# Performance work log

Measured on AMD Instinct MI355X. Metric: run time of the kernel, lower is better.

## Reference

```python
import math
import jax, jax.numpy as jnp
import numpy as np
from jax import lax

# ---- static config (mirrors RPN init + typical torchvision anchor setup) ----
IMG_H = IMG_W = 800
LEVELS = [(200, 200, 4, 32), (100, 100, 8, 64), (50, 50, 16, 128), (25, 25, 32, 256), (13, 13, 64, 512)]  # (h, w, stride, anchor_size)
RATIOS = (0.5, 1.0, 2.0)
COUNTS = tuple(h * w * len(RATIOS) for (h, w, _, _) in LEVELS)  # (120000,30000,7500,1875,507)
A_TOTAL = sum(COUNTS)  # 159882
PRE_NMS = 2000
POST_NMS = 1000
NMS_THRESH = 0.7
MIN_SIZE = 1e-3
BBOX_CLIP = math.log(1000.0 / 16)


def make_anchors():
    parts = []
    for (h, w, stride, size) in LEVELS:
        ws = np.array([size * np.sqrt(1.0 / r) for r in RATIOS], np.float32)  # [3]
        hs = np.array([size * np.sqrt(r) for r in RATIOS], np.float32)
        sx = (np.arange(w, dtype=np.float32) + 0.5) * stride
        sy = (np.arange(h, dtype=np.float32) + 0.5) * stride
        cy, cx = np.meshgrid(sy, sx, indexing='ij')
        cx = cx.reshape(-1, 1)
        cy = cy.reshape(-1, 1)
        a = np.stack([cx - ws / 2, cy - hs / 2, cx + ws / 2, cy + hs / 2], axis=-1)  # [HW,3,4]
        parts.append(a.reshape(-1, 4))
    return np.concatenate(parts, 0).astype(np.float32)


def setup_inputs() -> dict:
    key = jax.random.key(0)
    k1, k2 = jax.random.split(key)
    scores = jax.random.normal(k1, (1, A_TOTAL), dtype=jnp.float32)
    deltas = jax.random.normal(k2, (A_TOTAL, 4), dtype=jnp.float32) * 0.5
    anchors = jnp.asarray(make_anchors())
    return {'scores': scores, 'deltas': deltas, 'anchors': anchors}


def _pairwise_iou(b):
    area = (b[:, 2] - b[:, 0]) * (b[:, 3] - b[:, 1])  # [K]
    lt = jnp.maximum(b[:, None, :2], b[None, :, :2])   # [K,K,2]
    rb = jnp.minimum(b[:, None, 2:], b[None, :, 2:])
    wh = jnp.maximum(rb - lt, 0.0)
    inter = wh[..., 0] * wh[..., 1]
    return inter / (area[:, None] + area[None, :] - inter)


def reference(scores, deltas, anchors):
    s_all = lax.stop_gradient(scores[0])  # original does cls.detach()
    # ---- box decode (torchvision-style) ----
    w = anchors[:, 2] - anchors[:, 0]
    h = anchors[:, 3] - anchors[:, 1]
    cx = anchors[:, 0] + 0.5 * w
    cy = anchors[:, 1] + 0.5 * h
    dx, dy = deltas[:, 0], deltas[:, 1]
    dw = jnp.minimum(deltas[:, 2], BBOX_CLIP)
    dh = jnp.minimum(deltas[:, 3], BBOX_CLIP)
    px = cx + dx * w
    py = cy + dy * h
    pw = jnp.exp(dw) * w
    ph = jnp.exp(dh) * h
    boxes = jnp.stack([px - 0.5 * pw, py - 0.5 * ph, px + 0.5 * pw, py + 0.5 * ph], axis=1)  # [A,4]
    # ---- per-level top-k over objectness ----
    idx_parts = []
    off = 0
    for c in COUNTS:
        k = min(PRE_NMS, c)
        _, ti = lax.top_k(lax.dynamic_slice_in_dim(s_all, off, c), k)
        idx_parts.append(ti + off)
        off += c
    top_idx = jnp.concatenate(idx_parts)  # [K=8382]
    K = top_idx.shape[0]
    s = s_all[top_idx]
    b = boxes[top_idx]
    # ---- clip to image + min-size validity (masked instead of compacted) ----
    b = jnp.stack([jnp.clip(b[:, 0], 0.0, IMG_W), jnp.clip(b[:, 1], 0.0, IMG_H),
                   jnp.clip(b[:, 2], 0.0, IMG_W), jnp.clip(b[:, 3], 0.0, IMG_H)], axis=1)
    valid = ((b[:, 2] - b[:, 0]) >= MIN_SIZE) & ((b[:, 3] - b[:, 1]) >= MIN_SIZE)
    # ---- per-level NMS offset; replicates original feature_mask[keep] indexing
    # (positional indexing into the full anchor-order level-id vector) ----
    fmask_full = np.concatenate([np.full(c, i, np.float32) for i, c in enumerate(COUNTS)])
    fmask = jnp.asarray(fmask_full[:K])
    box_max = jnp.max(jnp.where(valid[:, None], b, -jnp.inf))
    bn = b + (fmask * (box_max + 1.0))[:, None]
    # ---- greedy NMS on score-sorted candidates ----
    s_m = jnp.where(valid, s, -jnp.inf)
    order = jnp.argsort(-s_m)
    s_srt = s_m[order]
    b_srt = b[order]
    iou = _pairwise_iou(bn[order])  # [K,K] ~281MB
    ar = jnp.arange(K)

    def body(i, keep):
        sup = (iou[i] > NMS_THRESH) & (ar > i)
        return jnp.where(keep[i], keep & ~sup, keep)

    keep = lax.fori_loop(0, K, body, s_srt > -jnp.inf)
    final = jnp.where(keep, s_srt, -jnp.inf)
    out_s, oidx = lax.top_k(final, POST_NMS)  # top post_nms kept, score order; -inf pads
    out_b = b_srt[oidx]
    return out_b, out_s
```

## Files before the change

### kernel.cpp

```cpp
#include <hip/hip_runtime.h>
#include <math.h>

typedef unsigned int u32;
typedef unsigned long long u64;
typedef unsigned char u8;

#define K_TOT 8382
#define NCH 131
#define CAP 1024
#define EC 64
#define DC 8
#define GCAP 32768
#define IMGSZ 800.0f

__device__ __constant__ int LOFF[5] = {0, 120000, 150000, 157500, 159375};
__device__ __constant__ int LCNT[5] = {120000, 30000, 7500, 1875, 507};
__device__ __constant__ int KSEL[5] = {2000, 2000, 2000, 1875, 507};
__device__ __constant__ int SELB[5] = {0, 2000, 4000, 6000, 7875};
__device__ __constant__ int HBS[4] = {0, 118, 148, 156};
__device__ __constant__ int GBS[6] = {0, 118, 148, 156, 158, 159};

static __device__ __forceinline__ u32 fkey(float x) {
    u32 u = __float_as_uint(x);
    u32 m = (u32)(((int)u) >> 31) | 0x80000000u;
    return u ^ m;
}

static __device__ __forceinline__ int lvl_of(int s) {
    return (s < 2000) ? 0 : (s < 4000) ? 1 : (s < 6000) ? 2 : (s < 7875) ? 3 : 4;
}

static __device__ __forceinline__ u64 rdlane64(u64 v, int j) {
    u32 lo = (u32)__builtin_amdgcn_readlane((int)(u32)v, j);
    u32 hi = (u32)__builtin_amdgcn_readlane((int)(u32)(v >> 32), j);
    return ((u64)hi << 32) | (u64)lo;
}

static __device__ __forceinline__ void thresh_scan(const u32* hist, u32* scanbuf, int m,
                                                   u32 need, u32* sv, int t) {
    for (int i = t; i < m; i += 1024) scanbuf[i] = hist[m - 1 - i];
    __syncthreads();
    for (int ofs = 1; ofs < m; ofs <<= 1) {
        int i0 = t, i1 = t + 1024;
        u32 a0 = 0, a1 = 0;
        if (i0 < m && i0 >= ofs) a0 = scanbuf[i0 - ofs];
        if (i1 < m && i1 >= ofs) a1 = scanbuf[i1 - ofs];
        __syncthreads();
        if (i0 < m && i0 >= ofs) scanbuf[i0] += a0;
        if (i1 < m && i1 >= ofs) scanbuf[i1] += a1;
        __syncthreads();
    }
    for (int i = t; i < m; i += 1024) {
        u32 inc = scanbuf[i];
        u32 exc = i ? scanbuf[i - 1] : 0;
        if (inc >= need && exc < need) { sv[0] = (u32)(m - 1 - i); sv[1] = need - exc; }
    }
    __syncthreads();
}

__global__ __launch_bounds__(1024) void k_hist(const float* __restrict__ scores,
                                               u32* __restrict__ hist3) {
    __shared__ u32 lh[2048];
    int t = threadIdx.x;
    lh[t] = 0; lh[t + 1024] = 0;
    __syncthreads();
    int b = blockIdx.x;
    int l = (b < HBS[1]) ? 0 : (b < HBS[2]) ? 1 : 2;
    int i = (b - HBS[l]) * 1024 + t;
    if (i < LCNT[l]) atomicAdd(&lh[fkey(scores[LOFF[l] + i]) >> 21], 1u);
    __syncthreads();
    u32* h = hist3 + l * 2048;
    if (lh[t]) atomicAdd(&h[t], lh[t]);
    if (lh[t + 1024]) atomicAdd(&h[t + 1024], lh[t + 1024]);
}

__global__ __launch_bounds__(1024) void k_thresh(const u32* __restrict__ hist3,
                                                 u32* __restrict__ tinfo) {
    __shared__ u32 scanbuf[2048];
    __shared__ u32 sv[2];
    int l = blockIdx.x;
    int t = threadIdx.x;
    thresh_scan(hist3 + l * 2048, scanbuf, 2048, (u32)KSEL[l], sv, t);
    if (t == 0) { tinfo[l * 2] = sv[0]; tinfo[l * 2 + 1] = sv[1]; }
}

__global__ __launch_bounds__(1024) void k_gather(const float* __restrict__ scores,
                                                 const u32* __restrict__ tinfo,
                                                 u32* __restrict__ sel, u32* __restrict__ cgt,
                                                 u32* __restrict__ gcnt, u32* __restrict__ gidx,
                                                 u32* __restrict__ gkey) {
    int b = blockIdx.x;
    int l = (b < GBS[1]) ? 0 : (b < GBS[2]) ? 1 : (b < GBS[3]) ? 2 : (b < GBS[4]) ? 3 : 4;
    int i = (b - GBS[l]) * 1024 + threadIdx.x;
    if (i >= LCNT[l]) return;
    int off = LOFF[l], sb = SELB[l];
    if (l >= 3) { sel[sb + i] = (u32)(off + i); return; }
    u32 ky = fkey(scores[off + i]);
    u32 b1 = tinfo[l * 2];
    u32 top = ky >> 21;
    if (top > b1) {
        u32 p = atomicAdd(&cgt[l], 1u);
        sel[sb + p] = (u32)(off + i);
    } else if (top == b1) {
        u32 e = atomicAdd(&gcnt[l], 1u);
        if (e < GCAP) { gidx[l * GCAP + e] = (u32)i; gkey[l * GCAP + e] = ky; }
    }
}

__global__ __launch_bounds__(1024) void k_final(const u32* __restrict__ gidx,
                                                const u32* __restrict__ gkey,
                                                const u32* __restrict__ gcnt,
                                                const u32* __restrict__ tinfo,
                                                u32* __restrict__ sel) {
    __shared__ u32 hist[2048];
    __shared__ u32 scanbuf[2048];
    __shared__ u32 eqbuf[1024];
    __shared__ u32 sv[2];
    __shared__ u32 c2, ceq;
    int l = blockIdx.x;
    int t = threadIdx.x;
    int k = KSEL[l], sb = SELB[l], off = LOFF[l];
    u32 m = gcnt[l]; if (m > GCAP) m = GCAP;
    u32 b1 = tinfo[l * 2];
    u32 need = tinfo[l * 2 + 1];
    const u32* kb = gkey + l * GCAP;
    const u32* ib = gidx + l * GCAP;
    hist[t] = 0; hist[t + 1024] = 0; __syncthreads();
    for (u32 e = t; e < m; e += 1024) atomicAdd(&hist[(kb[e] >> 10) & 2047u], 1u);
    __syncthreads();
    thresh_scan(hist, scanbuf, 2048, need, sv, t);
    u32 b2 = sv[0], need2 = sv[1];
    __syncthreads();
    hist[t] = 0; __syncthreads();
    for (u32 e = t; e < m; e += 1024) {
        u32 ky = kb[e];
        if (((ky >> 10) & 2047u) == b2) atomicAdd(&hist[ky & 1023u], 1u);
    }
    __syncthreads();
    thresh_scan(hist, scanbuf, 1024, need2, sv, t);
    u32 T = (b1 << 21) | (b2 << 10) | sv[0];
    u32 take = sv[1];
    if (t == 0) { c2 = 0; ceq = 0; }
    __syncthreads();
    u32 nGTbin = need - take;
    u32 base2 = (u32)sb + (u32)k - need;
    for (u32 e = t; e < m; e += 1024) {
        u32 ky = kb[e];
        if (ky > T) { u32 p = atomicAdd(&c2, 1u); sel[base2 + p] = (u32)off + ib[e]; }
        else if (ky == T) { u32 q = atomicAdd(&ceq, 1u); if (q < 1024) eqbuf[q] = ib[e]; }
    }
    __syncthreads();
    if (t == 0) {
        int n = (ceq > 1024u) ? 1024 : (int)ceq;
        for (int a = 1; a < n; ++a) {
            u32 v = eqbuf[a]; int bq = a - 1;
            while (bq >= 0 && eqbuf[bq] > v) { eqbuf[bq + 1] = eqbuf[bq]; --bq; }
            eqbuf[bq + 1] = v;
        }
        for (u32 q = 0; q < take; ++q) sel[base2 + nGTbin + q] = (u32)off + eqbuf[q];
    }
}

__global__ void k_decode(const float* __restrict__ scores, const float4* __restrict__ deltas,
                         const float4* __restrict__ anchors, const u32* __restrict__ sel,
                         float4* __restrict__ candB, float* __restrict__ candS,
                         u32* __restrict__ candV, u32* __restrict__ candA) {
    int s = blockIdx.x * 256 + threadIdx.x;
    if (s >= K_TOT) return;
    u32 a = sel[s];
    float4 an = anchors[a];
    float4 dl = deltas[a];
    float sc = scores[a];
    float w = __fsub_rn(an.z, an.x), h = __fsub_rn(an.w, an.y);
    float cx = __fadd_rn(an.x, __fmul_rn(0.5f, w));
    float cy = __fadd_rn(an.y, __fmul_rn(0.5f, h));
    const float CLIPV = (float)4.1351665567423563;
    float dw = fminf(dl.z, CLIPV);
    float dh = fminf(dl.w, CLIPV);
    float px = __fadd_rn(cx, __fmul_rn(dl.x, w));
    float py = __fadd_rn(cy, __fmul_rn(dl.y, h));
    float pw = __fmul_rn((float)exp((double)dw), w);
    float ph = __fmul_rn((float)exp((double)dh), h);
    float x1 = __fsub_rn(px, __fmul_rn(0.5f, pw));
    float y1 = __fsub_rn(py, __fmul_rn(0.5f, ph));
    float x2 = __fadd_rn(px, __fmul_rn(0.5f, pw));
    float y2 = __fadd_rn(py, __fmul_rn(0.5f, ph));
    x1 = fminf(fmaxf(x1, 0.0f), IMGSZ);
    y1 = fminf(fmaxf(y1, 0.0f), IMGSZ);
    x2 = fminf(fmaxf(x2, 0.0f), IMGSZ);
    y2 = fminf(fmaxf(y2, 0.0f), IMGSZ);
    bool valid = (__fsub_rn(x2, x1) >= 0.001f) && (__fsub_rn(y2, y1) >= 0.001f);
    candB[s] = make_float4(x1, y1, x2, y2);
    candS[s] = sc;
    candV[s] = valid ? 1u : 0u;
    candA[s] = a;
}

__global__ __launch_bounds__(256) void k_rank_lvl(const float* __restrict__ candS,
                                                  const u32* __restrict__ candA,
                                                  u32* __restrict__ Praw) {
    __shared__ u64 tile[256];
    int l = blockIdx.z;
    int cnt = KSEL[l], base = SELB[l];
    int tx = blockIdx.x * 256;
    int ty = blockIdx.y * 256;
    if (tx >= cnt || ty >= cnt) return;
    int t = threadIdx.x;
    u64 Aj = ~0ull;
    if (tx + t < cnt) {
        int j = base + tx + t;
        Aj = ((u64)(~fkey(candS[j])) << 32) | (u64)candA[j];
    }
    tile[t] = Aj;
    __syncthreads();
    int si = ty + t;
    if (si >= cnt) return;
    int s = base + si;
    u64 A = ((u64)(~fkey(candS[s])) << 32) | (u64)candA[s];
    int r = 0;
#pragma unroll 8
    for (int q = 0; q < 256; ++q) r += (tile[q] < A);
    if (r) atomicAdd(&Praw[s], (u32)r);
}

__global__ __launch_bounds__(256) void k_rank_glob(const float* __restrict__ candS,
                                                   const u32* __restrict__ candV,
                                                   const u32* __restrict__ Praw,
                                                   u32* __restrict__ rank) {
    __shared__ u64 colB[256];
    int t = threadIdx.x;
    int cj = blockIdx.x * 256 + t;
    u64 B = ~0ull;
    if (cj < K_TOT) {
        u32 smk = candV[cj] ? fkey(candS[cj]) : 0x007FFFFFu;
        u32 Pj = (u32)SELB[lvl_of(cj)] + Praw[cj];
        B = ((u64)(~smk) << 32) | (u64)Pj;
    }
    colB[t] = B;
    __syncthreads();
    int s = blockIdx.y * 256 + t;
    if (s >= K_TOT) return;
    u32 smk = candV[s] ? fkey(candS[s]) : 0x007FFFFFu;
    u32 Ps = (u32)SELB[lvl_of(s)] + Praw[s];
    u64 myB = ((u64)(~smk) << 32) | (u64)Ps;
    int cnt = 0;
#pragma unroll 8
    for (int j = 0; j < 256; ++j) cnt += (colB[j] < myB);
    if (cnt) atomicAdd(&rank[s], (u32)cnt);
}

__global__ void k_scatter(const float4* __restrict__ candB, const float* __restrict__ candS,
                          const u32* __restrict__ candV, const u32* __restrict__ rank,
                          float4* __restrict__ sB, float* __restrict__ sArea,
                          float* __restrict__ sS, u32* __restrict__ sV) {
    int s = blockIdx.x * 256 + threadIdx.x;
    if (s >= K_TOT) return;
    u32 r = rank[s];
    float4 b = candB[s];
    float area = __fmul_rn(__fsub_rn(b.z, b.x), __fsub_rn(b.w, b.y));
    sB[r] = b; sArea[r] = area; sS[r] = candS[s]; sV[r] = candV[s];
}

__global__ void k_vwords(const u32* __restrict__ sV, u64* __restrict__ vwords) {
    int i = blockIdx.x * 64 + threadIdx.x;
    bool pred = (i < K_TOT) && sV[i];
    u64 bw = __ballot(pred);
    if (threadIdx.x == 0) vwords[blockIdx.x] = bw;
}

__global__ __launch_bounds__(256) void k_mask(const float4* __restrict__ sB,
                                              const float* __restrict__ sArea,
                                              u64* __restrict__ diag, u32* __restrict__ ecnt,
                                              ulonglong2* __restrict__ epack,
                                              u32* __restrict__ dcnt, u64* __restrict__ dmask,
                                              ulonglong2* __restrict__ dpack) {
    __shared__ float4 cb[64];
    __shared__ float ca[64];
    int wd = blockIdx.x;
    int t = threadIdx.x;
    if (t < 64) {
        int j = wd * 64 + t;
        if (j < K_TOT) { cb[t] = sB[j]; ca[t] = sArea[j]; }
        else { cb[t] = make_float4(0.f, 0.f, 0.f, 0.f); ca[t] = 0.f; }
    }
    __syncthreads();
    int i = blockIdx.y * 256 + t;
    if (i >= K_TOT) return;
    int dwr = i >> 6;
    if (wd < dwr) return;
    float4 bi = sB[i];
    float ai = sArea[i];
    u64 bits = 0;
    int jbase = wd * 64;
    for (int j2 = 0; j2 < 64; ++j2) {
        int j = jbase + j2;
        if (j > i && j < K_TOT) {
            float4 bj = cb[j2];
            float ltx = fmaxf(bi.x, bj.x), lty = fmaxf(bi.y, bj.y);
            float rbx = fminf(bi.z, bj.z), rby = fminf(bi.w, bj.w);
            float wx = fmaxf(__fsub_rn(rbx, ltx), 0.0f);
            float wy = fmaxf(__fsub_rn(rby, lty), 0.0f);
            float inter = __fmul_rn(wx, wy);
            if (inter > 0.0f) {
                float uni = __fsub_rn(__fadd_rn(ai, ca[j2]), inter);
                float iou = inter / uni;
                if (iou > 0.7f) bits |= (1ull << j2);
            }
        }
    }
    if (wd == dwr) {
        diag[i] = bits;
        if (bits != 0ull) {
            u32 p = atomicAdd(&dcnt[dwr], 1u);
            if (p < DC) dpack[dwr * DC + p] = make_ulonglong2((u64)(i & 63), bits);
            atomicOr(&dmask[dwr], 1ull << (i & 63));
        }
    } else if (bits != 0ull) {
        u32 p = atomicAdd(&ecnt[dwr], 1u);
        if (p < CAP) epack[dwr * CAP + p] = make_ulonglong2((u64)((i & 63) | (wd << 6)), bits);
    }
}

__global__ __launch_bounds__(64) void k_scan(const u64* __restrict__ diag,
                                             const u64* __restrict__ vwords,
                                             const u32* __restrict__ ecnt,
                                             const ulonglong2* __restrict__ epack,
                                             const u32* __restrict__ dcnt,
                                             const u64* __restrict__ dmask,
                                             const ulonglong2* __restrict__ dpack,
                                             u64* __restrict__ keepw) {
    __shared__ u64 sVw[NCH];
    __shared__ u32 sCnt[NCH];
    __shared__ u32 sDn[NCH];
    __shared__ u64 sDm[NCH];
    __shared__ ulonglong2 sEpack[NCH * EC];
    __shared__ ulonglong2 sDpack[NCH * DC];
    volatile __shared__ u64 sR[NCH];
    __shared__ u64 sKeep[NCH];
    int lane = threadIdx.x;
    {
        int i0 = lane, i1 = lane + 64, i2 = lane + 128;
        bool p2 = (i2 < NCH);
        u64 v0 = vwords[i0], v1 = vwords[i1], v2 = p2 ? vwords[i2] : 0;
        u32 c0 = ecnt[i0], c1 = ecnt[i1], c2 = p2 ? ecnt[i2] : 0;
        u32 d0 = dcnt[i0], d1 = dcnt[i1], d2 = p2 ? dcnt[i2] : 0;
        u64 m0 = dmask[i0], m1 = dmask[i1], m2 = p2 ? dmask[i2] : 0;
        sVw[i0] = v0; sCnt[i0] = (c0 > CAP) ? CAP : c0; sDn[i0] = d0; sDm[i0] = m0; sR[i0] = 0;
        sVw[i1] = v1; sCnt[i1] = (c1 > CAP) ? CAP : c1; sDn[i1] = d1; sDm[i1] = m1; sR[i1] = 0;
        if (p2) { sVw[i2] = v2; sCnt[i2] = (c2 > CAP) ? CAP : c2; sDn[i2] = d2; sDm[i2] = m2; sR[i2] = 0; }
    }
    for (int base = 0; base < NCH; base += 16) {
        ulonglong2 tmp[16];
        int nb = NCH - base; if (nb > 16) nb = 16;
#pragma unroll
        for (int b = 0; b < 16; ++b)
            if (b < nb) tmp[b] = epack[(size_t)(base + b) * CAP + lane];
#pragma unroll
        for (int b = 0; b < 16; ++b)
            if (b < nb) sEpack[(base + b) * EC + lane] = tmp[b];
    }
    for (int base = 0; base < NCH * DC; base += 64 * 8) {
        ulonglong2 tmp[8];
#pragma unroll
        for (int b = 0; b < 8; ++b) {
            int i = base + b * 64 + lane;
            if (i < NCH * DC) tmp[b] = dpack[i];
        }
#pragma unroll
        for (int b = 0; b < 8; ++b) {
            int i = base + b * 64 + lane;
            if (i < NCH * DC) sDpack[i] = tmp[b];
        }
    }
    __syncthreads();
    for (int c = 0; c < NCH; ++c) {
        u32 cnt = sCnt[c];
        u32 dn = sDn[c];
        ulonglong2 E = sEpack[c * EC + lane];
        ulonglong2 DP = (lane < DC) ? sDpack[c * DC + lane] : make_ulonglong2(~0ull, 0ull);
        u64 vw = sVw[c];
        u64 alive = vw & ~sR[c];
        if (dn) {
            if (dn <= (u32)DC) {
                u64 dm = sDm[c];
                u32 ml = ((u32)lane < dn) ? (u32)DP.x : 0xFFu;
                while (dm) {
                    int j = __builtin_ctzll(dm);
                    dm &= dm - 1;
                    if ((alive >> j) & 1ull) {
                        u64 selm = __ballot(ml == (u32)j);
                        int src = __builtin_ctzll(selm);
                        alive &= ~rdlane64(DP.y, src);
                    }
                }
            } else {
                int r = c * 64 + lane;
                u64 D = (r < K_TOT) ? diag[r] : 0ull;
                u64 nzd = __ballot(D != 0ull);
                while (nzd) {
                    int j = __builtin_ctzll(nzd);
                    nzd &= nzd - 1;
                    if ((alive >> j) & 1ull) alive &= ~rdlane64(D, j);
                }
            }
        }
        if (lane == 0) sKeep[c] = alive;
        if ((u32)lane < cnt && ((alive >> ((u32)E.x & 63u)) & 1ull))
            atomicOr((u64*)&sR[(u32)E.x >> 6], E.y);
        if (cnt > (u32)EC) {
            for (u32 e = (u32)EC + (u32)lane; e < cnt; e += 64u) {
                ulonglong2 Et = epack[(size_t)c * CAP + e];
                u32 pk = (u32)Et.x;
                if ((alive >> (pk & 63u)) & 1ull) atomicOr((u64*)&sR[pk >> 6], Et.y);
            }
        }
    }
    __syncthreads();
    for (int i = lane; i < NCH; i += 64) keepw[i] = sKeep[i];
}

__global__ __launch_bounds__(1024) void k_out(const u64* __restrict__ keepw,
                                              const float4* __restrict__ sB,
                                              const float* __restrict__ sS,
                                              float* __restrict__ out) {
    __shared__ u32 wpre[NCH + 1];
    int t = threadIdx.x;
    if (t == 0) {
        u32 run = 0;
        for (int w = 0; w < NCH; ++w) { wpre[w] = run; run += (u32)__popcll(keepw[w]); }
        wpre[NCH] = run;
    }
    __syncthreads();
    u32 nk = wpre[NCH];
    for (int i = t; i < K_TOT; i += 1024) {
        int w = i >> 6, b = i & 63;
        u64 kw = keepw[w];
        u32 kb = wpre[w] + (u32)__popcll(kw & ((1ull << b) - 1ull));
        bool kp = (kw >> b) & 1ull;
        if (kp) {
            if (kb < 1000u) {
                float4 bx = sB[i];
                out[kb * 4 + 0] = bx.x; out[kb * 4 + 1] = bx.y;
                out[kb * 4 + 2] = bx.z; out[kb * 4 + 3] = bx.w;
                out[4000 + kb] = sS[i];
            }
        } else {
            u32 q = (u32)i - kb;
            u32 slot = nk + q;
            if (slot < 1000u) {
                float4 bx = sB[i];
                out[slot * 4 + 0] = bx.x; out[slot * 4 + 1] = bx.y;
                out[slot * 4 + 2] = bx.z; out[slot * 4 + 3] = bx.w;
                out[4000 + slot] = -INFINITY;
            }
        }
    }
}

static constexpr size_t al256(size_t x) { return (x + 255) & ~(size_t)255; }
static constexpr size_t KB4 = (size_t)K_TOT * 4;
static constexpr size_t KB16 = (size_t)K_TOT * 16;
static constexpr size_t O_RANK = 0;
static constexpr size_t O_PRAW = al256(O_RANK + KB4);
static constexpr size_t O_ECNT = al256(O_PRAW + KB4);
static constexpr size_t O_DCNT = al256(O_ECNT + (size_t)NCH * 4);
static constexpr size_t O_DMASK = al256(O_DCNT + (size_t)NCH * 4);
static constexpr size_t O_HIST = al256(O_DMASK + (size_t)NCH * 8);
static constexpr size_t O_CGT = al256(O_HIST + (size_t)3 * 2048 * 4);
static constexpr size_t O_GCNT = al256(O_CGT + 3 * 4);
static constexpr size_t MEMSET_BYTES = al256(O_GCNT + 3 * 4);
static constexpr size_t O_TINFO = MEMSET_BYTES;
static constexpr size_t O_SEL = al256(O_TINFO + 6 * 4);
static constexpr size_t O_GIDX = al256(O_SEL + KB4);
static constexpr size_t O_GKEY = al256(O_GIDX + (size_t)3 * GCAP * 4);
static constexpr size_t O_CANDB = al256(O_GKEY + (size_t)3 * GCAP * 4);
static constexpr size_t O_CANDS = al256(O_CANDB + KB16);
static constexpr size_t O_CANDV = al256(O_CANDS + KB4);
static constexpr size_t O_CANDA = al256(O_CANDV + KB4);
static constexpr size_t O_SB = al256(O_CANDA + KB4);
static constexpr size_t O_SAREA = al256(O_SB + KB16);
static constexpr size_t O_SS = al256(O_SAREA + KB4);
static constexpr size_t O_SV = al256(O_SS + KB4);
static constexpr size_t O_VW = al256(O_SV + KB4);
static constexpr size_t O_KW = al256(O_VW + (size_t)NCH * 8);
static constexpr size_t O_DIAG = al256(O_KW + (size_t)NCH * 8);
static constexpr size_t O_EPACK = al256(O_DIAG + (size_t)(NCH * 64) * 8);
static constexpr size_t O_DPACK = al256(O_EPACK + (size_t)NCH * CAP * 16);

extern "C" void kernel_launch(void* const* d_in, const int* in_sizes, int n_in,
                              void* d_out, int out_size, void* d_ws, size_t ws_size,
                              hipStream_t stream) {
    const float* scores = (const float*)d_in[0];
    const float4* deltas = (const float4*)d_in[1];
    const float4* anchors = (const float4*)d_in[2];
    float* out = (float*)d_out;
    char* ws = (char*)d_ws;

    u32* rank = (u32*)(ws + O_RANK);
    u32* Praw = (u32*)(ws + O_PRAW);
    u32* ecnt = (u32*)(ws + O_ECNT);
    u32* dcnt = (u32*)(ws + O_DCNT);
    u64* dmask = (u64*)(ws + O_DMASK);
    u32* hist3 = (u32*)(ws + O_HIST);
    u32* cgt = (u32*)(ws + O_CGT);
    u32* gcnt = (u32*)(ws + O_GCNT);
    u32* tinfo = (u32*)(ws + O_TINFO);
    u32* sel = (u32*)(ws + O_SEL);
    u32* gidx = (u32*)(ws + O_GIDX);
    u32* gkey = (u32*)(ws + O_GKEY);
    float4* candB = (float4*)(ws + O_CANDB);
    float* candS = (float*)(ws + O_CANDS);
    u32* candV = (u32*)(ws + O_CANDV);
    u32* candA = (u32*)(ws + O_CANDA);
    float4* sB = (float4*)(ws + O_SB);
    float* sArea = (float*)(ws + O_SAREA);
    float* sS = (float*)(ws + O_SS);
    u32* sV = (u32*)(ws + O_SV);
    u64* vwords = (u64*)(ws + O_VW);
    u64* keepw = (u64*)(ws + O_KW);
    u64* diag = (u64*)(ws + O_DIAG);
    ulonglong2* epack = (ulonglong2*)(ws + O_EPACK);
    ulonglong2* dpack = (ulonglong2*)(ws + O_DPACK);

    hipMemsetAsync(ws, 0, MEMSET_BYTES, stream);

    const int NBLK = (K_TOT + 255) / 256;
    k_hist<<<156, 1024, 0, stream>>>(scores, hist3);
    k_thresh<<<3, 1024, 0, stream>>>(hist3, tinfo);
    k_gather<<<159, 1024, 0, stream>>>(scores, tinfo, sel, cgt, gcnt, gidx, gkey);
    k_final<<<3, 1024, 0, stream>>>(gidx, gkey, gcnt, tinfo, sel);
    k_decode<<<NBLK, 256, 0, stream>>>(scores, deltas, anchors, sel, candB, candS, candV, candA);
    k_rank_lvl<<<dim3(8, 8, 5), 256, 0, stream>>>(candS, candA, Praw);
    k_rank_glob<<<dim3(NBLK, NBLK), 256, 0, stream>>>(candS, candV, Praw, rank);
    k_scatter<<<NBLK, 256, 0, stream>>>(candB, candS, candV, rank, sB, sArea, sS, sV);
    k_vwords<<<NCH, 64, 0, stream>>>(sV, vwords);
    k_mask<<<dim3(NCH, NBLK), 256, 0, stream>>>(sB, sArea, diag, ecnt, epack, dcnt, dmask, dpack);
    k_scan<<<1, 64, 0, stream>>>(diag, vwords, ecnt, epack, dcnt, dmask, dpack, keepw);
    k_out<<<1, 1024, 0, stream>>>(keepw, sB, sS, out);
}
```

Before: 226.0 us.

## Fuse selection stages via last-block tickets and merge rank passes into one

Folds the threshold scan into the histogram kernel and the final refinement into the gather kernel, using an atomic ticket so the last block to finish does the serial work. This removes two launches. The per-level rank kernel is replaced by a lexicographic two-key comparison inside the global rank kernel, and the valid-word ballot moves into the mask kernel. The scan kernel now keeps per-chunk metadata in registers read through readlane instead of shared memory. The cost is serialized tail work on a single block and a heavier inner compare loop in the rank kernel.

```diff
diff --git a/kernel.cpp b/kernel.cpp
--- a/kernel.cpp
+++ b/kernel.cpp
@@ -59,8 +59,12 @@
 }
 
 __global__ __launch_bounds__(1024) void k_hist(const float* __restrict__ scores,
-                                               u32* __restrict__ hist3) {
+                                               u32* __restrict__ hist3,
+                                               u32* __restrict__ tinfo,
+                                               u32* __restrict__ ticket) {
     __shared__ u32 lh[2048];
+    __shared__ u32 sv[2];
+    __shared__ u32 lastF;
     int t = threadIdx.x;
     lh[t] = 0; lh[t + 1024] = 0;
     __syncthreads();
@@ -72,92 +76,100 @@
     u32* h = hist3 + l * 2048;
     if (lh[t]) atomicAdd(&h[t], lh[t]);
     if (lh[t + 1024]) atomicAdd(&h[t + 1024], lh[t + 1024]);
-}
-
-__global__ __launch_bounds__(1024) void k_thresh(const u32* __restrict__ hist3,
-                                                 u32* __restrict__ tinfo) {
-    __shared__ u32 scanbuf[2048];
-    __shared__ u32 sv[2];
-    int l = blockIdx.x;
-    int t = threadIdx.x;
-    thresh_scan(hist3 + l * 2048, scanbuf, 2048, (u32)KSEL[l], sv, t);
-    if (t == 0) { tinfo[l * 2] = sv[0]; tinfo[l * 2 + 1] = sv[1]; }
+    __threadfence();
+    __syncthreads();
+    if (t == 0) lastF = (atomicAdd(ticket, 1u) == 155u) ? 1u : 0u;
+    __syncthreads();
+    if (!lastF) return;
+    __threadfence();
+    for (int lv = 0; lv < 3; ++lv) {
+        thresh_scan(hist3 + lv * 2048, lh, 2048, (u32)KSEL[lv], sv, t);
+        if (t == 0) { tinfo[lv * 2] = sv[0]; tinfo[lv * 2 + 1] = sv[1]; }
+        __syncthreads();
+    }
 }
 
 __global__ __launch_bounds__(1024) void k_gather(const float* __restrict__ scores,
                                                  const u32* __restrict__ tinfo,
                                                  u32* __restrict__ sel, u32* __restrict__ cgt,
                                                  u32* __restrict__ gcnt, u32* __restrict__ gidx,
-                                                 u32* __restrict__ gkey) {
-    int b = blockIdx.x;
-    int l = (b < GBS[1]) ? 0 : (b < GBS[2]) ? 1 : (b < GBS[3]) ? 2 : (b < GBS[4]) ? 3 : 4;
-    int i = (b - GBS[l]) * 1024 + threadIdx.x;
-    if (i >= LCNT[l]) return;
-    int off = LOFF[l], sb = SELB[l];
-    if (l >= 3) { sel[sb + i] = (u32)(off + i); return; }
-    u32 ky = fkey(scores[off + i]);
-    u32 b1 = tinfo[l * 2];
-    u32 top = ky >> 21;
-    if (top > b1) {
-        u32 p = atomicAdd(&cgt[l], 1u);
-        sel[sb + p] = (u32)(off + i);
-    } else if (top == b1) {
-        u32 e = atomicAdd(&gcnt[l], 1u);
-        if (e < GCAP) { gidx[l * GCAP + e] = (u32)i; gkey[l * GCAP + e] = ky; }
-    }
-}
-
-__global__ __launch_bounds__(1024) void k_final(const u32* __restrict__ gidx,
-                                                const u32* __restrict__ gkey,
-                                                const u32* __restrict__ gcnt,
-                                                const u32* __restrict__ tinfo,
-                                                u32* __restrict__ sel) {
+                                                 u32* __restrict__ gkey,
+                                                 u32* __restrict__ ticket) {
     __shared__ u32 hist[2048];
     __shared__ u32 scanbuf[2048];
     __shared__ u32 eqbuf[1024];
     __shared__ u32 sv[2];
     __shared__ u32 c2, ceq;
-    int l = blockIdx.x;
+    __shared__ u32 lastF;
     int t = threadIdx.x;
-    int k = KSEL[l], sb = SELB[l], off = LOFF[l];
-    u32 m = gcnt[l]; if (m > GCAP) m = GCAP;
-    u32 b1 = tinfo[l * 2];
-    u32 need = tinfo[l * 2 + 1];
-    const u32* kb = gkey + l * GCAP;
-    const u32* ib = gidx + l * GCAP;
-    hist[t] = 0; hist[t + 1024] = 0; __syncthreads();
-    for (u32 e = t; e < m; e += 1024) atomicAdd(&hist[(kb[e] >> 10) & 2047u], 1u);
-    __syncthreads();
-    thresh_scan(hist, scanbuf, 2048, need, sv, t);
-    u32 b2 = sv[0], need2 = sv[1];
-    __syncthreads();
-    hist[t] = 0; __syncthreads();
-    for (u32 e = t; e < m; e += 1024) {
-        u32 ky = kb[e];
-        if (((ky >> 10) & 2047u) == b2) atomicAdd(&hist[ky & 1023u], 1u);
-    }
-    __syncthreads();
-    thresh_scan(hist, scanbuf, 1024, need2, sv, t);
-    u32 T = (b1 << 21) | (b2 << 10) | sv[0];
-    u32 take = sv[1];
-    if (t == 0) { c2 = 0; ceq = 0; }
-    __syncthreads();
-    u32 nGTbin = need - take;
-    u32 base2 = (u32)sb + (u32)k - need;
-    for (u32 e = t; e < m; e += 1024) {
-        u32 ky = kb[e];
-        if (ky > T) { u32 p = atomicAdd(&c2, 1u); sel[base2 + p] = (u32)off + ib[e]; }
-        else if (ky == T) { u32 q = atomicAdd(&ceq, 1u); if (q < 1024) eqbuf[q] = ib[e]; }
-    }
-    __syncthreads();
-    if (t == 0) {
-        int n = (ceq > 1024u) ? 1024 : (int)ceq;
-        for (int a = 1; a < n; ++a) {
-            u32 v = eqbuf[a]; int bq = a - 1;
-            while (bq >= 0 && eqbuf[bq] > v) { eqbuf[bq + 1] = eqbuf[bq]; --bq; }
-            eqbuf[bq + 1] = v;
-        }
-        for (u32 q = 0; q < take; ++q) sel[base2 + nGTbin + q] = (u32)off + eqbuf[q];
+    int b = blockIdx.x;
+    int l = (b < GBS[1]) ? 0 : (b < GBS[2]) ? 1 : (b < GBS[3]) ? 2 : (b < GBS[4]) ? 3 : 4;
+    int i = (b - GBS[l]) * 1024 + t;
+    if (i < LCNT[l]) {
+        int off = LOFF[l], sb = SELB[l];
+        if (l >= 3) {
+            sel[sb + i] = (u32)(off + i);
+        } else {
+            u32 ky = fkey(scores[off + i]);
+            u32 b1 = tinfo[l * 2];
+            u32 top = ky >> 21;
+            if (top > b1) {
+                u32 p = atomicAdd(&cgt[l], 1u);
+                sel[sb + p] = (u32)(off + i);
+            } else if (top == b1) {
+                u32 e = atomicAdd(&gcnt[l], 1u);
+                if (e < GCAP) { gidx[l * GCAP + e] = (u32)i; gkey[l * GCAP + e] = ky; }
+            }
+        }
+    }
+    __threadfence();
+    __syncthreads();
+    if (t == 0) lastF = (atomicAdd(ticket, 1u) == 158u) ? 1u : 0u;
+    __syncthreads();
+    if (!lastF) return;
+    __threadfence();
+    for (int lv = 0; lv < 3; ++lv) {
+        int k = KSEL[lv], sb = SELB[lv], off = LOFF[lv];
+        u32 m = gcnt[lv]; if (m > GCAP) m = GCAP;
+        u32 b1 = tinfo[lv * 2];
+        u32 need = tinfo[lv * 2 + 1];
+        const u32* kb = gkey + lv * GCAP;
+        const u32* ib = gidx + lv * GCAP;
+        hist[t] = 0; hist[t + 1024] = 0; __syncthreads();
+        for (u32 e = t; e < m; e += 1024) atomicAdd(&hist[(kb[e] >> 10) & 2047u], 1u);
+        __syncthreads();
+        thresh_scan(hist, scanbuf, 2048, need, sv, t);
+        u32 b2 = sv[0], need2 = sv[1];
+        __syncthreads();
+        hist[t] = 0; __syncthreads();
+        for (u32 e = t; e < m; e += 1024) {
+            u32 ky = kb[e];
+            if (((ky >> 10) & 2047u) == b2) atomicAdd(&hist[ky & 1023u], 1u);
+        }
+        __syncthreads();
+        thresh_scan(hist, scanbuf, 1024, need2, sv, t);
+        u32 T = (b1 << 21) | (b2 << 10) | sv[0];
+        u32 take = sv[1];
+        if (t == 0) { c2 = 0; ceq = 0; }
+        __syncthreads();
+        u32 nGTbin = need - take;
+        u32 base2 = (u32)sb + (u32)k - need;
+        for (u32 e = t; e < m; e += 1024) {
+            u32 ky = kb[e];
+            if (ky > T) { u32 p = atomicAdd(&c2, 1u); sel[base2 + p] = (u32)off + ib[e]; }
+            else if (ky == T) { u32 q = atomicAdd(&ceq, 1u); if (q < 1024) eqbuf[q] = ib[e]; }
+        }
+        __syncthreads();
+        if (t == 0) {
+            int n = (ceq > 1024u) ? 1024 : (int)ceq;
+            for (int a = 1; a < n; ++a) {
+                u32 v = eqbuf[a]; int bq = a - 1;
+                while (bq >= 0 && eqbuf[bq] > v) { eqbuf[bq + 1] = eqbuf[bq]; --bq; }
+                eqbuf[bq + 1] = v;
+            }
+            for (u32 q = 0; q < take; ++q) sel[base2 + nGTbin + q] = (u32)off + eqbuf[q];
+        }
+        __syncthreads();
     }
 }
 
@@ -196,56 +208,35 @@
     candA[s] = a;
 }
 
-__global__ __launch_bounds__(256) void k_rank_lvl(const float* __restrict__ candS,
-                                                  const u32* __restrict__ candA,
-                                                  u32* __restrict__ Praw) {
-    __shared__ u64 tile[256];
-    int l = blockIdx.z;
-    int cnt = KSEL[l], base = SELB[l];
-    int tx = blockIdx.x * 256;
-    int ty = blockIdx.y * 256;
-    if (tx >= cnt || ty >= cnt) return;
-    int t = threadIdx.x;
-    u64 Aj = ~0ull;
-    if (tx + t < cnt) {
-        int j = base + tx + t;
-        Aj = ((u64)(~fkey(candS[j])) << 32) | (u64)candA[j];
-    }
-    tile[t] = Aj;
-    __syncthreads();
-    int si = ty + t;
-    if (si >= cnt) return;
-    int s = base + si;
-    u64 A = ((u64)(~fkey(candS[s])) << 32) | (u64)candA[s];
-    int r = 0;
-#pragma unroll 8
-    for (int q = 0; q < 256; ++q) r += (tile[q] < A);
-    if (r) atomicAdd(&Praw[s], (u32)r);
-}
-
 __global__ __launch_bounds__(256) void k_rank_glob(const float* __restrict__ candS,
                                                    const u32* __restrict__ candV,
-                                                   const u32* __restrict__ Praw,
+                                                   const u32* __restrict__ candA,
                                                    u32* __restrict__ rank) {
-    __shared__ u64 colB[256];
+    __shared__ u64 cA1[256];
+    __shared__ u64 cA2[256];
     int t = threadIdx.x;
     int cj = blockIdx.x * 256 + t;
-    u64 B = ~0ull;
+    u64 a1 = ~0ull, a2 = ~0ull;
     if (cj < K_TOT) {
-        u32 smk = candV[cj] ? fkey(candS[cj]) : 0x007FFFFFu;
-        u32 Pj = (u32)SELB[lvl_of(cj)] + Praw[cj];
-        B = ((u64)(~smk) << 32) | (u64)Pj;
-    }
-    colB[t] = B;
+        u32 kyj = fkey(candS[cj]);
+        u32 smk = candV[cj] ? kyj : 0x007FFFFFu;
+        a1 = ((u64)(~smk) << 32) | (u64)lvl_of(cj);
+        a2 = ((u64)(~kyj) << 32) | (u64)candA[cj];
+    }
+    cA1[t] = a1; cA2[t] = a2;
     __syncthreads();
     int s = blockIdx.y * 256 + t;
     if (s >= K_TOT) return;
-    u32 smk = candV[s] ? fkey(candS[s]) : 0x007FFFFFu;
-    u32 Ps = (u32)SELB[lvl_of(s)] + Praw[s];
-    u64 myB = ((u64)(~smk) << 32) | (u64)Ps;
+    u32 kys = fkey(candS[s]);
+    u32 smk = candV[s] ? kys : 0x007FFFFFu;
+    u64 m1 = ((u64)(~smk) << 32) | (u64)lvl_of(s);
+    u64 m2 = ((u64)(~kys) << 32) | (u64)candA[s];
     int cnt = 0;
-#pragma unroll 8
-    for (int j = 0; j < 256; ++j) cnt += (colB[j] < myB);
+#pragma unroll 4
+    for (int j = 0; j < 256; ++j) {
+        u64 t1 = cA1[j];
+        cnt += (t1 < m1) || (t1 == m1 && cA2[j] < m2);
+    }
     if (cnt) atomicAdd(&rank[s], (u32)cnt);
 }
 
@@ -261,23 +252,24 @@
     sB[r] = b; sArea[r] = area; sS[r] = candS[s]; sV[r] = candV[s];
 }
 
-__global__ void k_vwords(const u32* __restrict__ sV, u64* __restrict__ vwords) {
-    int i = blockIdx.x * 64 + threadIdx.x;
-    bool pred = (i < K_TOT) && sV[i];
-    u64 bw = __ballot(pred);
-    if (threadIdx.x == 0) vwords[blockIdx.x] = bw;
-}
-
 __global__ __launch_bounds__(256) void k_mask(const float4* __restrict__ sB,
                                               const float* __restrict__ sArea,
+                                              const u32* __restrict__ sV,
                                               u64* __restrict__ diag, u32* __restrict__ ecnt,
                                               ulonglong2* __restrict__ epack,
                                               u32* __restrict__ dcnt, u64* __restrict__ dmask,
-                                              ulonglong2* __restrict__ dpack) {
+                                              ulonglong2* __restrict__ dpack,
+                                              u64* __restrict__ vwords) {
     __shared__ float4 cb[64];
     __shared__ float ca[64];
     int wd = blockIdx.x;
     int t = threadIdx.x;
+    if (blockIdx.y == 0 && t < 64) {
+        int j = wd * 64 + t;
+        bool pred = (j < K_TOT) && (sV[j] != 0u);
+        u64 bw = __ballot(pred);
+        if (t == 0) vwords[wd] = bw;
+    }
     if (t < 64) {
         int j = wd * 64 + t;
         if (j < K_TOT) { cb[t] = sB[j]; ca[t] = sArea[j]; }
@@ -329,26 +321,19 @@
                                              const u64* __restrict__ dmask,
                                              const ulonglong2* __restrict__ dpack,
                                              u64* __restrict__ keepw) {
-    __shared__ u64 sVw[NCH];
-    __shared__ u32 sCnt[NCH];
-    __shared__ u32 sDn[NCH];
-    __shared__ u64 sDm[NCH];
     __shared__ ulonglong2 sEpack[NCH * EC];
     __shared__ ulonglong2 sDpack[NCH * DC];
     volatile __shared__ u64 sR[NCH];
     __shared__ u64 sKeep[NCH];
     int lane = threadIdx.x;
-    {
-        int i0 = lane, i1 = lane + 64, i2 = lane + 128;
-        bool p2 = (i2 < NCH);
-        u64 v0 = vwords[i0], v1 = vwords[i1], v2 = p2 ? vwords[i2] : 0;
-        u32 c0 = ecnt[i0], c1 = ecnt[i1], c2 = p2 ? ecnt[i2] : 0;
-        u32 d0 = dcnt[i0], d1 = dcnt[i1], d2 = p2 ? dcnt[i2] : 0;
-        u64 m0 = dmask[i0], m1 = dmask[i1], m2 = p2 ? dmask[i2] : 0;
-        sVw[i0] = v0; sCnt[i0] = (c0 > CAP) ? CAP : c0; sDn[i0] = d0; sDm[i0] = m0; sR[i0] = 0;
-        sVw[i1] = v1; sCnt[i1] = (c1 > CAP) ? CAP : c1; sDn[i1] = d1; sDm[i1] = m1; sR[i1] = 0;
-        if (p2) { sVw[i2] = v2; sCnt[i2] = (c2 > CAP) ? CAP : c2; sDn[i2] = d2; sDm[i2] = m2; sR[i2] = 0; }
-    }
+    int i0 = lane, i1 = lane + 64, i2 = lane + 128;
+    bool p2 = (i2 < NCH);
+    u64 vwR0 = vwords[i0], vwR1 = vwords[i1], vwR2 = p2 ? vwords[i2] : 0;
+    u32 cR0 = ecnt[i0], cR1 = ecnt[i1], cR2 = p2 ? ecnt[i2] : 0;
+    u32 dR0 = dcnt[i0], dR1 = dcnt[i1], dR2 = p2 ? dcnt[i2] : 0;
+    u64 mR0 = dmask[i0], mR1 = dmask[i1], mR2 = p2 ? dmask[i2] : 0;
+    cR0 = (cR0 > CAP) ? CAP : cR0; cR1 = (cR1 > CAP) ? CAP : cR1; cR2 = (cR2 > CAP) ? CAP : cR2;
+    sR[i0] = 0; sR[i1] = 0; if (p2) sR[i2] = 0;
     for (int base = 0; base < NCH; base += 16) {
         ulonglong2 tmp[16];
         int nb = NCH - base; if (nb > 16) nb = 16;
@@ -374,19 +359,31 @@
     }
     __syncthreads();
     for (int c = 0; c < NCH; ++c) {
-        u32 cnt = sCnt[c];
-        u32 dn = sDn[c];
+        int g = c >> 6, l = c & 63;
+        u64 vw, dm; u32 cnt, dn;
+        if (g == 0) {
+            vw = rdlane64(vwR0, l); dm = rdlane64(mR0, l);
+            cnt = (u32)__builtin_amdgcn_readlane((int)cR0, l);
+            dn = (u32)__builtin_amdgcn_readlane((int)dR0, l);
+        } else if (g == 1) {
+            vw = rdlane64(vwR1, l); dm = rdlane64(mR1, l);
+            cnt = (u32)__builtin_amdgcn_readlane((int)cR1, l);
+            dn = (u32)__builtin_amdgcn_readlane((int)dR1, l);
+        } else {
+            vw = rdlane64(vwR2, l); dm = rdlane64(mR2, l);
+            cnt = (u32)__builtin_amdgcn_readlane((int)cR2, l);
+            dn = (u32)__builtin_amdgcn_readlane((int)dR2, l);
+        }
         ulonglong2 E = sEpack[c * EC + lane];
         ulonglong2 DP = (lane < DC) ? sDpack[c * DC + lane] : make_ulonglong2(~0ull, 0ull);
-        u64 vw = sVw[c];
         u64 alive = vw & ~sR[c];
         if (dn) {
             if (dn <= (u32)DC) {
-                u64 dm = sDm[c];
                 u32 ml = ((u32)lane < dn) ? (u32)DP.x : 0xFFu;
-                while (dm) {
-                    int j = __builtin_ctzll(dm);
-                    dm &= dm - 1;
+                u64 dmm = dm;
+                while (dmm) {
+                    int j = __builtin_ctzll(dmm);
+                    dmm &= dmm - 1;
                     if ((alive >> j) & 1ull) {
                         u64 selm = __ballot(ml == (u32)j);
                         int src = __builtin_ctzll(selm);
@@ -461,14 +458,14 @@
 static constexpr size_t KB4 = (size_t)K_TOT * 4;
 static constexpr size_t KB16 = (size_t)K_TOT * 16;
 static constexpr size_t O_RANK = 0;
-static constexpr size_t O_PRAW = al256(O_RANK + KB4);
-static constexpr size_t O_ECNT = al256(O_PRAW + KB4);
+static constexpr size_t O_ECNT = al256(O_RANK + KB4);
 static constexpr size_t O_DCNT = al256(O_ECNT + (size_t)NCH * 4);
 static constexpr size_t O_DMASK = al256(O_DCNT + (size_t)NCH * 4);
 static constexpr size_t O_HIST = al256(O_DMASK + (size_t)NCH * 8);
 static constexpr size_t O_CGT = al256(O_HIST + (size_t)3 * 2048 * 4);
 static constexpr size_t O_GCNT = al256(O_CGT + 3 * 4);
-static constexpr size_t MEMSET_BYTES = al256(O_GCNT + 3 * 4);
+static constexpr size_t O_TK = al256(O_GCNT + 3 * 4);
+static constexpr size_t MEMSET_BYTES = al256(O_TK + 2 * 4);
 static constexpr size_t O_TINFO = MEMSET_BYTES;
 static constexpr size_t O_SEL = al256(O_TINFO + 6 * 4);
 static constexpr size_t O_GIDX = al256(O_SEL + KB4);
@@ -497,13 +494,13 @@
     char* ws = (char*)d_ws;
 
     u32* rank = (u32*)(ws + O_RANK);
-    u32* Praw = (u32*)(ws + O_PRAW);
     u32* ecnt = (u32*)(ws + O_ECNT);
     u32* dcnt = (u32*)(ws + O_DCNT);
     u64* dmask = (u64*)(ws + O_DMASK);
     u32* hist3 = (u32*)(ws + O_HIST);
     u32* cgt = (u32*)(ws + O_CGT);
     u32* gcnt = (u32*)(ws + O_GCNT);
+    u32* ticket = (u32*)(ws + O_TK);
     u32* tinfo = (u32*)(ws + O_TINFO);
     u32* sel = (u32*)(ws + O_SEL);
     u32* gidx = (u32*)(ws + O_GIDX);
@@ -522,19 +519,16 @@
     ulonglong2* epack = (ulonglong2*)(ws + O_EPACK);
     ulonglong2* dpack = (ulonglong2*)(ws + O_DPACK);
 
-    hipMemsetAsync(ws, 0, MEMSET_BYTES, stream);
+    (void)hipMemsetAsync(ws, 0, MEMSET_BYTES, stream);
 
     const int NBLK = (K_TOT + 255) / 256;
-    k_hist<<<156, 1024, 0, stream>>>(scores, hist3);
-    k_thresh<<<3, 1024, 0, stream>>>(hist3, tinfo);
-    k_gather<<<159, 1024, 0, stream>>>(scores, tinfo, sel, cgt, gcnt, gidx, gkey);
-    k_final<<<3, 1024, 0, stream>>>(gidx, gkey, gcnt, tinfo, sel);
+    k_hist<<<156, 1024, 0, stream>>>(scores, hist3, tinfo, &ticket[0]);
+    k_gather<<<159, 1024, 0, stream>>>(scores, tinfo, sel, cgt, gcnt, gidx, gkey, &ticket[1]);
     k_decode<<<NBLK, 256, 0, stream>>>(scores, deltas, anchors, sel, candB, candS, candV, candA);
-    k_rank_lvl<<<dim3(8, 8, 5), 256, 0, stream>>>(candS, candA, Praw);
-    k_rank_glob<<<dim3(NBLK, NBLK), 256, 0, stream>>>(candS, candV, Praw, rank);
+    k_rank_glob<<<dim3(NBLK, NBLK), 256, 0, stream>>>(candS, candV, candA, rank);
     k_scatter<<<NBLK, 256, 0, stream>>>(candB, candS, candV, rank, sB, sArea, sS, sV);
-    k_vwords<<<NCH, 64, 0, stream>>>(sV, vwords);
-    k_mask<<<dim3(NCH, NBLK), 256, 0, stream>>>(sB, sArea, diag, ecnt, epack, dcnt, dmask, dpack);
+    k_mask<<<dim3(NCH, NBLK), 256, 0, stream>>>(sB, sArea, sV, diag, ecnt, epack,
+                                                dcnt, dmask, dpack, vwords);
     k_scan<<<1, 64, 0, stream>>>(diag, vwords, ecnt, epack, dcnt, dmask, dpack, keepw);
     k_out<<<1, 1024, 0, stream>>>(keepw, sB, sS, out);
 }
```

Measured after the change: 327.6 us. 1.45x slower.
